# Kernel optimization log

Measured on AMD Instinct MI355X. Metric: run time of the kernel, lower is better.

## Reference

```python
import jax, jax.numpy as jnp
import numpy as np

NX = 768
N_HEAD = 12
N_CTX = 2048
BATCH = 4
EPS = 1e-5
NEG = -1000000000.0


def _layernorm(x, g, b):
    # NOTE: faithful to source bug: returns g + normalized + b (additive, not scale)
    u = jnp.mean(x, axis=-1, keepdims=True)
    s = jnp.mean((x - u) ** 2, axis=-1, keepdims=True)
    return g + (x - u) / jnp.sqrt(s + EPS) + b


def setup_inputs() -> dict:
    key = jax.random.key(0)
    ks = jax.random.split(key, 8)
    std = 0.02
    x = jax.random.normal(ks[0], (BATCH, N_CTX, NX), dtype=jnp.float32)
    w_attn = jax.random.normal(ks[1], (NX, 3 * NX), dtype=jnp.float32) * std
    b_attn = jnp.zeros((3 * NX,), jnp.float32)
    w_proj = jax.random.normal(ks[2], (NX, NX), dtype=jnp.float32) * std
    b_proj = jnp.zeros((NX,), jnp.float32)
    ln1_g = jnp.ones((NX,), jnp.float32)
    ln1_b = jnp.zeros((NX,), jnp.float32)
    w_fc = jax.random.normal(ks[3], (NX, 4 * NX), dtype=jnp.float32) * std
    b_fc = jnp.zeros((4 * NX,), jnp.float32)
    w_fc2 = jax.random.normal(ks[4], (4 * NX, NX), dtype=jnp.float32) * std
    b_fc2 = jnp.zeros((NX,), jnp.float32)
    ln2_g = jnp.ones((NX,), jnp.float32)
    ln2_b = jnp.zeros((NX,), jnp.float32)
    return dict(x=x, w_attn=w_attn, b_attn=b_attn, w_proj=w_proj, b_proj=b_proj,
                ln1_g=ln1_g, ln1_b=ln1_b, w_fc=w_fc, b_fc=b_fc,
                w_fc2=w_fc2, b_fc2=b_fc2, ln2_g=ln2_g, ln2_b=ln2_b)


def reference(x, w_attn, b_attn, w_proj, b_proj, ln1_g, ln1_b,
              w_fc, b_fc, w_fc2, b_fc2, ln2_g, ln2_b):
    B, S, D = x.shape
    dh = D // N_HEAD
    # --- attention (scale=False: no 1/sqrt(d)) ---
    qkv = x @ w_attn + b_attn                      # [B,S,3D]
    q, k, v = jnp.split(qkv, 3, axis=-1)
    q = q.reshape(B, S, N_HEAD, dh).transpose(0, 2, 1, 3)   # [B,H,S,dh]
    k = k.reshape(B, S, N_HEAD, dh).transpose(0, 2, 3, 1)   # [B,H,dh,S]
    v = v.reshape(B, S, N_HEAD, dh).transpose(0, 2, 1, 3)   # [B,H,S,dh]
    w = jnp.einsum('bhsd,bhdt->bhst', q, k)        # [B,H,S,S]
    mask = jnp.tril(jnp.ones((S, S), x.dtype))[None, None]
    w = w * mask + NEG * (1.0 - mask)
    w = jax.nn.softmax(w, axis=-1)
    a = jnp.einsum('bhst,bhtd->bhsd', w, v)        # [B,H,S,dh]
    a = a.transpose(0, 2, 1, 3).reshape(B, S, D)
    a = a @ w_proj + b_proj
    # dropout layers are identity (eval mode)
    n = _layernorm(x + a, ln1_g, ln1_b)
    # --- MLP (intended ReLU; source's nn.ReLU usage is a bug) ---
    h = jax.nn.relu(n @ w_fc + b_fc)
    m = h @ w_fc2 + b_fc2
    return _layernorm(n + m, ln2_g, ln2_b)
```

## Files before the change

kernel.cpp:

```cpp
#include <hip/hip_runtime.h>
#include <stdint.h>

#define NX 768
#define SEQ 2048
#define NHEAD 12
#define MROWS 8192
#define LN_EPS 1e-5f
#define MASK_NEG -1000000000.0f

typedef __bf16 bf16x8 __attribute__((ext_vector_type(8)));
typedef float f32x4 __attribute__((ext_vector_type(4)));

#define AS3(p)  ((__attribute__((address_space(3))) void*)(p))
#define AS1C(p) ((const __attribute__((address_space(1))) void*)(p))

__device__ __forceinline__ unsigned short f2bf(float f) {
  union { float f; unsigned int u; } v; v.f = f;
  unsigned int r = v.u + 0x7fffu + ((v.u >> 16) & 1u);
  return (unsigned short)(r >> 16);
}
__device__ __forceinline__ unsigned int f2bf_fast_u(float f) {
  union { float f; unsigned int u; } v; v.f = f;
  return (v.u + 0x8000u) >> 16;
}
__device__ __forceinline__ float bf2f(unsigned short u) {
  union { unsigned int u; float f; } v; v.u = ((unsigned int)u) << 16;
  return v.f;
}

__global__ void convert_f32_bf16(const float* __restrict__ in,
                                 unsigned short* __restrict__ out, int n4) {
  int i = blockIdx.x * blockDim.x + threadIdx.x;
  if (i >= n4) return;
  float4 v = ((const float4*)in)[i];
  ushort4 o;
  o.x = f2bf(v.x); o.y = f2bf(v.y); o.z = f2bf(v.z); o.w = f2bf(v.w);
  ((ushort4*)out)[i] = o;
}

__global__ void transpose_w(const float* __restrict__ w,
                            unsigned short* __restrict__ wt, int K, int N) {
  __shared__ float tile[32][33];
  int n0 = blockIdx.x * 32, k0 = blockIdx.y * 32;
  int tx = threadIdx.x, ty = threadIdx.y;
#pragma unroll
  for (int j = 0; j < 4; ++j)
    tile[ty + j * 8][tx] = w[(long)(k0 + ty + j * 8) * N + n0 + tx];
  __syncthreads();
#pragma unroll
  for (int j = 0; j < 4; ++j)
    wt[(long)(n0 + ty + j * 8) * K + k0 + tx] = f2bf(tile[tx][ty + j * 8]);
}

__global__ void transpose_v(const unsigned short* __restrict__ qkv,
                            unsigned short* __restrict__ vt) {
  __shared__ unsigned short tile[64][68];
  int s0 = blockIdx.x * 64;
  int bh = blockIdx.y, b = bh / NHEAD, h = bh % NHEAD;
  int tx = threadIdx.x, ty = threadIdx.y;
  const unsigned short* src = qkv + (long)b * SEQ * 2304 + 1536 + h * 64;
#pragma unroll
  for (int j = 0; j < 4; ++j) {
    int s = ty + j * 16;
    ushort4 vv = *(const ushort4*)(src + (long)(s0 + s) * 2304 + tx * 4);
    *(ushort4*)(&tile[s][tx * 4]) = vv;
  }
  __syncthreads();
  unsigned short* dst = vt + (long)bh * 64 * SEQ + s0;
#pragma unroll
  for (int j = 0; j < 4; ++j) {
    int d = ty + j * 16;
    ushort4 o;
    o.x = tile[tx * 4 + 0][d]; o.y = tile[tx * 4 + 1][d];
    o.z = tile[tx * 4 + 2][d]; o.w = tile[tx * 4 + 3][d];
    *(ushort4*)(dst + (long)d * SEQ + tx * 4) = o;
  }
}

template <int ACT, int BN>
__global__ __launch_bounds__(256) void gemm_bt(const unsigned short* __restrict__ A,
                                               const unsigned short* __restrict__ Bt,
                                               const float* __restrict__ bias,
                                               unsigned short* __restrict__ C,
                                               int Nsz, int K) {
  constexpr int ABUF = 128 * 64;
  constexpr int BBUF = BN * 64;
  constexpr int BUF = ABUF + BBUF;
  __shared__ __align__(16) unsigned short smem[2 * BUF];
  const int tid = threadIdx.x;
  const int w = tid >> 6, lane = tid & 63;
  const int l15 = lane & 15, quad = lane >> 4;
  constexpr int MT = (BN == 128) ? 4 : 2;
  const int wrow0 = (BN == 128) ? (w >> 1) * 64 : w * 32;
  const int wcol0 = (BN == 128) ? (w & 1) * 64 : 0;
  const long m0 = (long)blockIdx.x * 128;
  const long n0 = (long)blockIdx.y * BN;

  const int srow = tid >> 3;
  const int sg = tid & 7;

  auto stage = [&](int kb) {
    unsigned short* As = smem + (kb & 1) * BUF;
    unsigned short* Bs = As + ABUF;
    const int k0 = kb * 64;
#pragma unroll
    for (int p = 0; p < 4; ++p) {
      int row = p * 32 + srow;
      int g = sg ^ (row & 7);
      const unsigned short* gA = A + (m0 + row) * (long)K + k0 + g * 8;
      __builtin_amdgcn_global_load_lds(AS1C(gA), AS3(As + p * 2048 + w * 512), 16, 0, 0);
    }
#pragma unroll
    for (int p = 0; p < BN / 32; ++p) {
      int row = p * 32 + srow;
      int g = sg ^ (row & 7);
      const unsigned short* gB = Bt + (n0 + row) * (long)K + k0 + g * 8;
      __builtin_amdgcn_global_load_lds(AS1C(gB), AS3(Bs + p * 2048 + w * 512), 16, 0, 0);
    }
  };

  f32x4 acc[MT][4] = {};
  const int nkb = K / 64;

  stage(0);
  for (int kb = 0; kb < nkb; ++kb) {
    __syncthreads();
    if (kb + 1 < nkb) stage(kb + 1);
    const unsigned short* As = smem + (kb & 1) * BUF;
    const unsigned short* Bs = As + ABUF;
#pragma unroll
    for (int s2 = 0; s2 < 2; ++s2) {
      const int phys = ((s2 * 4 + quad) ^ (l15 & 7)) * 8;
      bf16x8 af[MT], bfr[4];
#pragma unroll
      for (int mt = 0; mt < MT; ++mt)
        af[mt] = *(const bf16x8*)(As + (wrow0 + mt * 16 + l15) * 64 + phys);
#pragma unroll
      for (int nt = 0; nt < 4; ++nt)
        bfr[nt] = *(const bf16x8*)(Bs + (wcol0 + nt * 16 + l15) * 64 + phys);
#pragma unroll
      for (int mt = 0; mt < MT; ++mt)
#pragma unroll
        for (int nt = 0; nt < 4; ++nt)
          acc[mt][nt] = __builtin_amdgcn_mfma_f32_16x16x32_bf16(af[mt], bfr[nt], acc[mt][nt], 0, 0, 0);
    }
  }
  __syncthreads();

  unsigned short* Ew = smem + w * (16 * 72);
  const long gmB = m0 + wrow0;
  const long gnB = n0 + wcol0;
  float bv[4];
#pragma unroll
  for (int nt = 0; nt < 4; ++nt) bv[nt] = bias[gnB + nt * 16 + l15];
  const int prow = lane >> 3, pcol = (lane & 7) * 8;
#pragma unroll
  for (int mt = 0; mt < MT; ++mt) {
#pragma unroll
    for (int nt = 0; nt < 4; ++nt)
#pragma unroll
      for (int r = 0; r < 4; ++r) {
        float v = acc[mt][nt][r] + bv[nt];
        if (ACT == 1) v = fmaxf(v, 0.f);
        Ew[(quad * 4 + r) * 72 + nt * 16 + l15] = f2bf(v);
      }
#pragma unroll
    for (int ps = 0; ps < 2; ++ps) {
      int row = ps * 8 + prow;
      int4 t = *(const int4*)(Ew + row * 72 + pcol);
      *(int4*)(C + (gmB + mt * 16 + row) * (long)Nsz + gnB + pcol) = t;
    }
  }
}

__global__ __launch_bounds__(256) void attn_v6(const unsigned short* __restrict__ qkv,
                                               const unsigned short* __restrict__ vt,
                                               unsigned short* __restrict__ out) {
  const int blk = blockIdx.x;
  const int bh = blk >> 4;
  const int bx = blk & 15;
  const int b = bh / NHEAD, h = bh % NHEAD;
  const int tid = threadIdx.x;
  const int w = tid >> 6, lane = tid & 63, l15 = lane & 15, quad = lane >> 4;

  __shared__ __align__(16) unsigned short Ks[2][64 * 64];
  __shared__ __align__(16) unsigned short Vs[2][64 * 64];
  __shared__ __align__(16) unsigned short Ps[4][16 * 64];

  const long rowbase = (long)b * SEQ;
  unsigned short* Pw = &Ps[w][0];
  const unsigned short* vbh = vt + (long)bh * 64 * SEQ;
  const float LOG2E = 1.4426950408889634f;

  const int krow = tid >> 3;
  const int kgo = (((tid & 7) ^ (krow & 7)) * 8);
  const unsigned short* kbase = qkv + rowbase * 2304L + 768 + h * 64;

  for (int pass = 0; pass < 2; ++pass) {
    const int qt = (pass == 0) ? bx : 31 - bx;
    const int niter = qt + 1;
    const int qrow = qt * 64 + w * 16 + l15;
    const int qg = qrow;

    bf16x8 qf[2];
#pragma unroll
    for (int s2 = 0; s2 < 2; ++s2) {
      int4 raw = *(const int4*)(qkv + (rowbase + qrow) * 2304L + h * 64 + s2 * 32 + quad * 8);
      const unsigned short* rp = (const unsigned short*)&raw;
#pragma unroll
      for (int j = 0; j < 8; ++j)
        qf[s2][j] = (__bf16)(bf2f(rp[j]) * LOG2E);
    }

    const unsigned short* kp[2];
    const unsigned short* vp[2];
#pragma unroll
    for (int p = 0; p < 2; ++p) {
      kp[p] = kbase + (long)(p * 32 + krow) * 2304 + kgo;
      vp[p] = vbh + (long)(p * 32 + krow) * SEQ + kgo;
    }

    float l_sum = 0.f;
    f32x4 o_acc[4] = {};

    __syncthreads();
#pragma unroll
    for (int p = 0; p < 2; ++p) {
      __builtin_amdgcn_global_load_lds(AS1C(kp[p]), AS3(&Ks[0][0] + p * 2048 + w * 512), 16, 0, 0);
      __builtin_amdgcn_global_load_lds(AS1C(vp[p]), AS3(&Vs[0][0] + p * 2048 + w * 512), 16, 0, 0);
      kp[p] += 64 * 2304;
      vp[p] += 64;
    }

    for (int it = 0; it < niter; ++it) {
      __syncthreads();
      if (it + 1 < niter) {
        const int nb = (it + 1) & 1;
#pragma unroll
        for (int p = 0; p < 2; ++p) {
          __builtin_amdgcn_global_load_lds(AS1C(kp[p]), AS3(&Ks[nb][0] + p * 2048 + w * 512), 16, 0, 0);
          __builtin_amdgcn_global_load_lds(AS1C(vp[p]), AS3(&Vs[nb][0] + p * 2048 + w * 512), 16, 0, 0);
          kp[p] += 64 * 2304;
          vp[p] += 64;
        }
      }
      const unsigned short* Kc = &Ks[it & 1][0];
      const unsigned short* Vc = &Vs[it & 1][0];

      f32x4 st[4] = {};
#pragma unroll
      for (int nt = 0; nt < 4; ++nt) {
        int key = nt * 16 + l15;
#pragma unroll
        for (int s2 = 0; s2 < 2; ++s2) {
          int phys = (s2 * 4 + quad) ^ (key & 7);
          bf16x8 kf = *(const bf16x8*)(Kc + key * 64 + phys * 8);
          st[nt] = __builtin_amdgcn_mfma_f32_16x16x32_bf16(kf, qf[s2], st[nt], 0, 0, 0);
        }
      }

      if (it == niter - 1) {
#pragma unroll
        for (int nt = 0; nt < 4; ++nt) {
          int kg = it * 64 + nt * 16 + quad * 4;
#pragma unroll
          for (int r = 0; r < 4; ++r)
            if (kg + r > qg) st[nt][r] = MASK_NEG;
        }
      }

      float psum = 0.f;
#pragma unroll
      for (int nt = 0; nt < 4; ++nt)
#pragma unroll
        for (int r = 0; r < 4; ++r) {
          float p = __builtin_amdgcn_exp2f(st[nt][r]);
          st[nt][r] = p;
          psum += p;
        }
      psum += __shfl_xor(psum, 16);
      psum += __shfl_xor(psum, 32);
      l_sum += psum;

#pragma unroll
      for (int nt = 0; nt < 4; ++nt) {
        unsigned int lo = f2bf_fast_u(st[nt][0]) | (f2bf_fast_u(st[nt][1]) << 16);
        unsigned int hi = f2bf_fast_u(st[nt][2]) | (f2bf_fast_u(st[nt][3]) << 16);
        int g8 = (nt * 2 + (quad >> 1)) ^ (l15 & 7);
        uint2 pv; pv.x = lo; pv.y = hi;
        *(uint2*)(Pw + l15 * 64 + g8 * 8 + (quad & 1) * 4) = pv;
      }

#pragma unroll
      for (int c = 0; c < 2; ++c) {
        int phys = ((c * 4 + quad) ^ (l15 & 7)) * 8;
        bf16x8 pf = *(const bf16x8*)(Pw + l15 * 64 + phys);
#pragma unroll
        for (int ntd = 0; ntd < 4; ++ntd) {
          int d = ntd * 16 + l15;
          bf16x8 vf = *(const bf16x8*)(Vc + d * 64 + phys);
          o_acc[ntd] = __builtin_amdgcn_mfma_f32_16x16x32_bf16(pf, vf, o_acc[ntd], 0, 0, 0);
        }
      }
    }

#pragma unroll
    for (int r = 0; r < 4; ++r) {
      float lq = __shfl(l_sum, quad * 4 + r);
      float inv = 1.f / lq;
      int q = qt * 64 + w * 16 + quad * 4 + r;
#pragma unroll
      for (int ntd = 0; ntd < 4; ++ntd) {
        int d = ntd * 16 + l15;
        out[(rowbase + q) * (long)NX + h * 64 + d] = f2bf(o_acc[ntd][r] * inv);
      }
    }
  }
}

__global__ __launch_bounds__(256) void add_ln(const float* __restrict__ x_f,
                                              const unsigned short* __restrict__ x_b,
                                              const unsigned short* __restrict__ y_b,
                                              const float* __restrict__ g,
                                              const float* __restrict__ beta,
                                              float* __restrict__ out_f,
                                              unsigned short* __restrict__ out_b) {
  const int row = blockIdx.x, t = threadIdx.x;
  const long base = (long)row * NX;
  float v[3];
#pragma unroll
  for (int j = 0; j < 3; ++j) {
    int i = t + j * 256;
    float a = x_f ? x_f[base + i] : bf2f(x_b[base + i]);
    v[j] = a + bf2f(y_b[base + i]);
  }
  __shared__ float red[4];
  int wv = t >> 6, ln = t & 63;

  float ssum = v[0] + v[1] + v[2];
#pragma unroll
  for (int sh = 32; sh >= 1; sh >>= 1) ssum += __shfl_xor(ssum, sh);
  if (ln == 0) red[wv] = ssum;
  __syncthreads();
  float u = (red[0] + red[1] + red[2] + red[3]) * (1.f / NX);
  __syncthreads();

  float d0 = v[0] - u, d1 = v[1] - u, d2 = v[2] - u;
  float sq = d0 * d0 + d1 * d1 + d2 * d2;
#pragma unroll
  for (int sh = 32; sh >= 1; sh >>= 1) sq += __shfl_xor(sq, sh);
  if (ln == 0) red[wv] = sq;
  __syncthreads();
  float s = (red[0] + red[1] + red[2] + red[3]) * (1.f / NX);
  float rinv = rsqrtf(s + LN_EPS);

  float dd[3] = {d0, d1, d2};
#pragma unroll
  for (int j = 0; j < 3; ++j) {
    int i = t + j * 256;
    float o = g[i] + dd[j] * rinv + beta[i];
    if (out_f) out_f[base + i] = o;
    else out_b[base + i] = f2bf(o);
  }
}

extern "C" void kernel_launch(void* const* d_in, const int* in_sizes, int n_in,
                              void* d_out, int out_size, void* d_ws, size_t ws_size,
                              hipStream_t stream) {
  const float* x      = (const float*)d_in[0];
  const float* w_attn = (const float*)d_in[1];
  const float* b_attn = (const float*)d_in[2];
  const float* w_proj = (const float*)d_in[3];
  const float* b_proj = (const float*)d_in[4];
  const float* ln1_g  = (const float*)d_in[5];
  const float* ln1_b  = (const float*)d_in[6];
  const float* w_fc   = (const float*)d_in[7];
  const float* b_fc   = (const float*)d_in[8];
  const float* w_fc2  = (const float*)d_in[9];
  const float* b_fc2  = (const float*)d_in[10];
  const float* ln2_g  = (const float*)d_in[11];
  const float* ln2_b  = (const float*)d_in[12];
  float* out = (float*)d_out;

  char* ws = (char*)d_ws;
  size_t off = 0;
  auto alloc = [&](size_t bytes) {
    char* p = ws + off;
    off += (bytes + 255) & ~(size_t)255;
    return p;
  };
  unsigned short* xb      = (unsigned short*)alloc((size_t)MROWS * NX * 2);
  unsigned short* wt_attn = (unsigned short*)alloc((size_t)2304 * 768 * 2);
  unsigned short* wt_proj = (unsigned short*)alloc((size_t)768 * 768 * 2);
  unsigned short* wt_fc   = (unsigned short*)alloc((size_t)3072 * 768 * 2);
  unsigned short* wt_fc2  = (unsigned short*)alloc((size_t)768 * 3072 * 2);
  unsigned short* qkv     = (unsigned short*)alloc((size_t)MROWS * 3072 * 2);
  unsigned short* hbuf    = qkv;
  unsigned short* abuf    = (unsigned short*)alloc((size_t)MROWS * NX * 2);
  unsigned short* mbuf    = abuf;
  unsigned short* nbuf    = (unsigned short*)alloc((size_t)MROWS * NX * 2);
  unsigned short* vtb     = nbuf;
  unsigned short* pout    = xb;

  convert_f32_bf16<<<(MROWS * NX / 4 + 255) / 256, 256, 0, stream>>>(x, xb, MROWS * NX / 4);
  transpose_w<<<dim3(2304 / 32, 768 / 32), dim3(32, 8), 0, stream>>>(w_attn, wt_attn, 768, 2304);
  transpose_w<<<dim3(768 / 32, 768 / 32), dim3(32, 8), 0, stream>>>(w_proj, wt_proj, 768, 768);
  transpose_w<<<dim3(3072 / 32, 768 / 32), dim3(32, 8), 0, stream>>>(w_fc, wt_fc, 768, 3072);
  transpose_w<<<dim3(768 / 32, 3072 / 32), dim3(32, 8), 0, stream>>>(w_fc2, wt_fc2, 3072, 768);

  gemm_bt<0, 128><<<dim3(MROWS / 128, 2304 / 128), 256, 0, stream>>>(xb, wt_attn, b_attn, qkv, 2304, 768);
  transpose_v<<<dim3(SEQ / 64, 48), dim3(16, 16), 0, stream>>>(qkv, vtb);
  attn_v6<<<768, 256, 0, stream>>>(qkv, vtb, abuf);
  gemm_bt<0, 64><<<dim3(MROWS / 128, 768 / 64), 256, 0, stream>>>(abuf, wt_proj, b_proj, pout, 768, 768);
  add_ln<<<MROWS, 256, 0, stream>>>(x, nullptr, pout, ln1_g, ln1_b, nullptr, nbuf);
  gemm_bt<1, 128><<<dim3(MROWS / 128, 3072 / 128), 256, 0, stream>>>(nbuf, wt_fc, b_fc, hbuf, 3072, 768);
  gemm_bt<0, 64><<<dim3(MROWS / 128, 768 / 64), 256, 0, stream>>>(hbuf, wt_fc2, b_fc2, mbuf, 768, 3072);
  add_ln<<<MROWS, 256, 0, stream>>>(nullptr, nbuf, mbuf, ln2_g, ln2_b, out, nullptr);
}
```

Before: 354.8 us.

## Precompute GEMM staging pointers, remap attention blocks, narrow QKV GEMM tile

The GEMM staging loop now computes its swizzled global row pointers once and advances them by 64 elements per k-block, instead of recomputing the address math on every stage. The attention kernel remaps block indices so that 8 consecutive blocks cover different batch-heads, which spreads work across CUs and may improve K/V cache locality. The QKV projection switches to the BN=64 tile variant, doubling the grid for better occupancy and load balance at the cost of less reuse of A per block. Per-thread pointer registers rise slightly.

```diff
diff --git a/kernel.cpp b/kernel.cpp
--- a/kernel.cpp
+++ b/kernel.cpp
@@ -99,23 +99,31 @@
   const int srow = tid >> 3;
   const int sg = tid & 7;
 
+  const unsigned short* ap[4];
+#pragma unroll
+  for (int p = 0; p < 4; ++p) {
+    int row = p * 32 + srow;
+    ap[p] = A + (m0 + row) * (long)K + (sg ^ (row & 7)) * 8;
+  }
+  const unsigned short* bp[BN / 32];
+#pragma unroll
+  for (int p = 0; p < BN / 32; ++p) {
+    int row = p * 32 + srow;
+    bp[p] = Bt + (n0 + row) * (long)K + (sg ^ (row & 7)) * 8;
+  }
+
   auto stage = [&](int kb) {
     unsigned short* As = smem + (kb & 1) * BUF;
     unsigned short* Bs = As + ABUF;
-    const int k0 = kb * 64;
 #pragma unroll
     for (int p = 0; p < 4; ++p) {
-      int row = p * 32 + srow;
-      int g = sg ^ (row & 7);
-      const unsigned short* gA = A + (m0 + row) * (long)K + k0 + g * 8;
-      __builtin_amdgcn_global_load_lds(AS1C(gA), AS3(As + p * 2048 + w * 512), 16, 0, 0);
+      __builtin_amdgcn_global_load_lds(AS1C(ap[p]), AS3(As + p * 2048 + w * 512), 16, 0, 0);
+      ap[p] += 64;
     }
 #pragma unroll
     for (int p = 0; p < BN / 32; ++p) {
-      int row = p * 32 + srow;
-      int g = sg ^ (row & 7);
-      const unsigned short* gB = Bt + (n0 + row) * (long)K + k0 + g * 8;
-      __builtin_amdgcn_global_load_lds(AS1C(gB), AS3(Bs + p * 2048 + w * 512), 16, 0, 0);
+      __builtin_amdgcn_global_load_lds(AS1C(bp[p]), AS3(Bs + p * 2048 + w * 512), 16, 0, 0);
+      bp[p] += 64;
     }
   };
 
@@ -173,12 +181,14 @@
   }
 }
 
-__global__ __launch_bounds__(256) void attn_v6(const unsigned short* __restrict__ qkv,
+__global__ __launch_bounds__(256) void attn_v7(const unsigned short* __restrict__ qkv,
                                                const unsigned short* __restrict__ vt,
                                                unsigned short* __restrict__ out) {
   const int blk = blockIdx.x;
-  const int bh = blk >> 4;
-  const int bx = blk & 15;
+  const int bh_lo = blk & 7;
+  const int j = blk >> 3;
+  const int bx = j & 15;
+  const int bh = (j >> 4) * 8 + bh_lo;
   const int b = bh / NHEAD, h = bh % NHEAD;
   const int tid = threadIdx.x;
   const int w = tid >> 6, lane = tid & 63, l15 = lane & 15, quad = lane >> 4;
@@ -208,8 +218,8 @@
       int4 raw = *(const int4*)(qkv + (rowbase + qrow) * 2304L + h * 64 + s2 * 32 + quad * 8);
       const unsigned short* rp = (const unsigned short*)&raw;
 #pragma unroll
-      for (int j = 0; j < 8; ++j)
-        qf[s2][j] = (__bf16)(bf2f(rp[j]) * LOG2E);
+      for (int j2 = 0; j2 < 8; ++j2)
+        qf[s2][j2] = (__bf16)(bf2f(rp[j2]) * LOG2E);
     }
 
     const unsigned short* kp[2];
@@ -408,9 +418,9 @@
   transpose_w<<<dim3(3072 / 32, 768 / 32), dim3(32, 8), 0, stream>>>(w_fc, wt_fc, 768, 3072);
   transpose_w<<<dim3(768 / 32, 3072 / 32), dim3(32, 8), 0, stream>>>(w_fc2, wt_fc2, 3072, 768);
 
-  gemm_bt<0, 128><<<dim3(MROWS / 128, 2304 / 128), 256, 0, stream>>>(xb, wt_attn, b_attn, qkv, 2304, 768);
+  gemm_bt<0, 64><<<dim3(MROWS / 128, 2304 / 64), 256, 0, stream>>>(xb, wt_attn, b_attn, qkv, 2304, 768);
   transpose_v<<<dim3(SEQ / 64, 48), dim3(16, 16), 0, stream>>>(qkv, vtb);
-  attn_v6<<<768, 256, 0, stream>>>(qkv, vtb, abuf);
+  attn_v7<<<768, 256, 0, stream>>>(qkv, vtb, abuf);
   gemm_bt<0, 64><<<dim3(MROWS / 128, 768 / 64), 256, 0, stream>>>(abuf, wt_proj, b_proj, pout, 768, 768);
   add_ln<<<MROWS, 256, 0, stream>>>(x, nullptr, pout, ln1_g, ln1_b, nullptr, nbuf);
   gemm_bt<1, 128><<<dim3(MROWS / 128, 3072 / 128), 256, 0, stream>>>(nbuf, wt_fc, b_fc, hbuf, 3072, 768);
```

Measured after the change: 341.4 us. 1.04x faster.
